# Optimization experiments

Measured on AMD Instinct MI355X. Metric: run time of the kernel, lower is better.

## Reference

```python
import jax, jax.numpy as jnp
import numpy as np

B, N, C, H, AD, HID = 2, 1024, 768, 12, 8, 3072
SCALE = (C // H) ** -0.5


def setup_inputs() -> dict:
    key = jax.random.key(0)
    ks = jax.random.split(key, 32)
    inp = {}
    for i in range(5):
        inp[f"x{i}"] = jax.random.normal(ks[i], (B, N, C), jnp.float32)
    def w(i, shape, s=0.02):
        return jax.random.normal(ks[i], shape, jnp.float32) * s
    inp.update({
        "ln1_g": jnp.ones((C,), jnp.float32), "ln1_b": jnp.zeros((C,), jnp.float32),
        "ln2_g": jnp.ones((C,), jnp.float32), "ln2_b": jnp.zeros((C,), jnp.float32),
        "qkv_w": w(5, (C, 3 * C)), "qkv_b": jnp.zeros((3 * C,), jnp.float32),
        "proj_w": w(6, (C, C)), "proj_b": jnp.zeros((C,), jnp.float32),
        "fc1_w": w(7, (C, HID)), "fc1_b": jnp.zeros((HID,), jnp.float32),
        "fc2_w": w(8, (HID, C)), "fc2_b": jnp.zeros((C,), jnp.float32),
        "at_dw": w(9, (C, AD)), "at_db": jnp.zeros((AD,), jnp.float32),
        "at_mw": w(10, (AD, AD)), "at_mb": jnp.zeros((AD,), jnp.float32),
        "at_uw": w(11, (AD, C)), "at_ub": jnp.zeros((C,), jnp.float32),
        "a2_dw": w(12, (C, AD)), "a2_db": jnp.zeros((AD,), jnp.float32),
        "a2_mw": w(13, (AD, AD)), "a2_mb": jnp.zeros((AD,), jnp.float32),
        "a2_uw": w(14, (AD, C)), "a2_ub": jnp.zeros((C,), jnp.float32),
    })
    return inp


def _ln(x, g, b, eps=1e-5):
    mu = x.mean(-1, keepdims=True)
    xc = x - mu
    var = (xc * xc).mean(-1, keepdims=True)
    return xc * jax.lax.rsqrt(var + eps) * g + b


def _adapter(x, dw, db, mw, mb, uw, ub):
    h = x @ dw + db          # bottleneck down [., AD]
    h = h @ mw + mb          # mid
    return h @ uw + ub       # up back to C


def _attn(x, qkv_w, qkv_b, proj_w, proj_b):
    # x: [S, B, N, C] (streams folded in leading axis)
    s, b, n, c = x.shape
    qkv = (x @ qkv_w + qkv_b).reshape(s, b, n, 3, H, c // H)
    q, k, v = jnp.moveaxis(qkv, 3, 0)            # each [S,B,N,H,D]
    scores = jnp.einsum('sbnhd,sbmhd->sbhnm', q * SCALE, k)  # fp32; clamp is a no-op
    p = jax.nn.softmax(scores, axis=-1)
    o = jnp.einsum('sbhnm,sbmhd->sbnhd', p, v).reshape(s, b, n, c)
    return o @ proj_w + proj_b


def reference(x0, x1, x2, x3, x4,
              ln1_g, ln1_b, ln2_g, ln2_b,
              qkv_w, qkv_b, proj_w, proj_b,
              fc1_w, fc1_b, fc2_w, fc2_b,
              at_dw, at_db, at_mw, at_mb, at_uw, at_ub,
              a2_dw, a2_db, a2_mw, a2_mb, a2_uw, a2_ub):
    xs = jnp.stack([x0, x1, x2, x3, x4])          # [5,B,N,C]
    n1 = _ln(xs, ln1_g, ln1_b)
    a1 = _adapter(n1, at_dw, at_db, at_mw, at_mb, at_uw, at_ub)
    ao = _attn(n1, qkv_w, qkv_b, proj_w, proj_b)
    # cross-stream residuals: x01=a1[0], x12=a1[1], ..., x10=a1[1], x21=a1[2], ...
    y0 = xs[0] + ao[0] + a1[1]
    y1 = xs[1] + ao[1] + a1[0] + a1[2]
    y2 = xs[2] + ao[2] + a1[1] + a1[3]
    y3 = xs[3] + ao[3] + a1[2] + a1[4]
    y4 = xs[4] + ao[4] + a1[3]
    ys = jnp.stack([y0, y1, y2, y3, y4])
    a2 = _adapter(_ln(ys, ln1_g, ln1_b), a2_dw, a2_db, a2_mw, a2_mb, a2_uw, a2_ub)
    h = _ln(ys, ln2_g, ln2_b) @ fc1_w + fc1_b
    m = jax.nn.gelu(h, approximate=False) @ fc2_w + fc2_b
    z0 = ys[0] + m[0] + a2[1]
    z1 = ys[1] + m[1] + a2[0] + a2[2]
    z2 = ys[2] + m[2] + a2[1] + a2[3]
    z3 = ys[3] + m[3] + a2[2] + a2[4]
    z4 = ys[4] + m[4] + a2[3]
    return jnp.stack([z0, z1, z2, z3, z4])        # [5,B,N,C]
```

## Files before the change

kernel.cpp:

```cpp
#include <hip/hip_runtime.h>
#include <math.h>

typedef __bf16 bf16;
typedef __attribute__((ext_vector_type(8))) __bf16 bf16x8;
typedef __attribute__((ext_vector_type(4))) __bf16 bf16x4;
typedef __attribute__((ext_vector_type(4))) float f32x4;
typedef __attribute__((ext_vector_type(16))) float f32x16;

#define TOK   10240
#define CD    768
#define NQKV  2304
#define NHID  3072
#define SEQ   1024
#define NH    12

__device__ __forceinline__ f32x4 mfma16(bf16x8 a, bf16x8 b, f32x4 c) {
  return __builtin_amdgcn_mfma_f32_16x16x32_bf16(a, b, c, 0, 0, 0);
}
__device__ __forceinline__ f32x16 mfma32(bf16x8 a, bf16x8 b, f32x16 c) {
  return __builtin_amdgcn_mfma_f32_32x32x16_bf16(a, b, c, 0, 0, 0);
}

__device__ __forceinline__ void gload16(const void* g, void* l) {
  __builtin_amdgcn_global_load_lds(
      (const __attribute__((address_space(1))) void*)g,
      (__attribute__((address_space(3))) void*)l, 16, 0, 0);
}

__device__ __forceinline__ unsigned pack2(bf16 a, bf16 b) {
  union { unsigned short u[2]; unsigned v; } x;
  x.u[0] = __builtin_bit_cast(unsigned short, a);
  x.u[1] = __builtin_bit_cast(unsigned short, b);
  return x.v;
}

__global__ __launch_bounds__(256) void transpose_to_bf16(
    const float* __restrict__ in, bf16* __restrict__ out, int K, int N) {
  __shared__ float tile[32][33];
  const int bn = blockIdx.x * 32, bk = blockIdx.y * 32;
  const int r = threadIdx.x >> 5, c = threadIdx.x & 31;
#pragma unroll
  for (int i = 0; i < 4; ++i)
    tile[r + 8 * i][c] = in[(size_t)(bk + r + 8 * i) * N + bn + c];
  __syncthreads();
#pragma unroll
  for (int i = 0; i < 4; ++i)
    out[(size_t)(bn + r + 8 * i) * K + bk + c] = (bf16)tile[c][r + 8 * i];
}

__global__ __launch_bounds__(256) void ln5_kernel(
    const float* __restrict__ x0, const float* __restrict__ x1,
    const float* __restrict__ x2, const float* __restrict__ x3,
    const float* __restrict__ x4, const float* __restrict__ g,
    const float* __restrict__ b, bf16* __restrict__ out) {
  const int w = threadIdx.x >> 6, lane = threadIdx.x & 63;
  const int row = blockIdx.x * 4 + w;
  const int s = row >> 11, rem = row & 2047;
  const float* xp;
  switch (s) {
    case 0: xp = x0; break; case 1: xp = x1; break; case 2: xp = x2; break;
    case 3: xp = x3; break; default: xp = x4; break;
  }
  const f32x4* xr = (const f32x4*)(xp + (size_t)rem * CD);
  f32x4 v[3];
#pragma unroll
  for (int i = 0; i < 3; ++i) v[i] = xr[lane + 64 * i];
  float sum = 0.f;
#pragma unroll
  for (int i = 0; i < 3; ++i)
#pragma unroll
    for (int j = 0; j < 4; ++j) sum += v[i][j];
#pragma unroll
  for (int m = 32; m >= 1; m >>= 1) sum += __shfl_xor(sum, m);
  const float mu = sum * (1.f / 768.f);
  float vs = 0.f;
#pragma unroll
  for (int i = 0; i < 3; ++i)
#pragma unroll
    for (int j = 0; j < 4; ++j) { float d = v[i][j] - mu; vs += d * d; }
#pragma unroll
  for (int m = 32; m >= 1; m >>= 1) vs += __shfl_xor(vs, m);
  const float rstd = rsqrtf(vs * (1.f / 768.f) + 1e-5f);
  const f32x4* gp = (const f32x4*)g;
  const f32x4* bp = (const f32x4*)b;
  bf16* orow = out + (size_t)row * CD;
#pragma unroll
  for (int i = 0; i < 3; ++i) {
    const int c4 = lane + 64 * i;
    f32x4 gg = gp[c4], bb = bp[c4];
    bf16x4 o;
#pragma unroll
    for (int j = 0; j < 4; ++j)
      o[j] = (bf16)((v[i][j] - mu) * rstd * gg[j] + bb[j]);
    *(bf16x4*)(orow + c4 * 4) = o;
  }
}

__global__ __launch_bounds__(256) void ln_dual_kernel(
    const float* __restrict__ in, const float* __restrict__ g1,
    const float* __restrict__ b1, const float* __restrict__ g2,
    const float* __restrict__ b2, bf16* __restrict__ o1,
    bf16* __restrict__ o2) {
  const int w = threadIdx.x >> 6, lane = threadIdx.x & 63;
  const int row = blockIdx.x * 4 + w;
  const f32x4* xr = (const f32x4*)(in + (size_t)row * CD);
  f32x4 v[3];
#pragma unroll
  for (int i = 0; i < 3; ++i) v[i] = xr[lane + 64 * i];
  float sum = 0.f;
#pragma unroll
  for (int i = 0; i < 3; ++i)
#pragma unroll
    for (int j = 0; j < 4; ++j) sum += v[i][j];
#pragma unroll
  for (int m = 32; m >= 1; m >>= 1) sum += __shfl_xor(sum, m);
  const float mu = sum * (1.f / 768.f);
  float vs = 0.f;
#pragma unroll
  for (int i = 0; i < 3; ++i)
#pragma unroll
    for (int j = 0; j < 4; ++j) { float d = v[i][j] - mu; vs += d * d; }
#pragma unroll
  for (int m = 32; m >= 1; m >>= 1) vs += __shfl_xor(vs, m);
  const float rstd = rsqrtf(vs * (1.f / 768.f) + 1e-5f);
  bf16* r1 = o1 + (size_t)row * CD;
  bf16* r2 = o2 + (size_t)row * CD;
#pragma unroll
  for (int i = 0; i < 3; ++i) {
    const int c4 = lane + 64 * i;
    f32x4 gg1 = ((const f32x4*)g1)[c4], bb1 = ((const f32x4*)b1)[c4];
    f32x4 gg2 = ((const f32x4*)g2)[c4], bb2 = ((const f32x4*)b2)[c4];
    bf16x4 oa, ob;
#pragma unroll
    for (int j = 0; j < 4; ++j) {
      float n = (v[i][j] - mu) * rstd;
      oa[j] = (bf16)(n * gg1[j] + bb1[j]);
      ob[j] = (bf16)(n * gg2[j] + bb2[j]);
    }
    *(bf16x4*)(r1 + c4 * 4) = oa;
    *(bf16x4*)(r2 + c4 * 4) = ob;
  }
}

template <int EPI>
__global__ __launch_bounds__(256) void gemm_bt(
    const bf16* __restrict__ A, const bf16* __restrict__ Bt,
    const float* __restrict__ bias, void* __restrict__ Cout, int N, int K) {
  __shared__ bf16 As[4096];
  __shared__ bf16 Bs[4096];
  const int t = threadIdx.x, lane = t & 63, w = t >> 6;
  const int wm = w >> 1, wn = w & 1;
  const int bn = blockIdx.x, bm = blockIdx.y;
  f32x4 acc[4][4] = {};

  const int srow = t >> 2;
  const int scol = ((t & 3) ^ (srow & 3)) << 3;
  const bf16* a0 = A + (size_t)(bm * 128 + srow) * K + scol;
  const bf16* b0 = Bt + (size_t)(bn * 128 + srow) * K + scol;
  bf16* asw = As + w * 512;
  bf16* bsw = Bs + w * 512;
  const size_t rstride = (size_t)64 * K;

  const int arow = wm * 64 + (lane & 15);
  const int brow = wn * 64 + (lane & 15);
  const int pch = (((lane >> 4) ^ (lane & 3)) << 3);

  for (int kt = 0; kt < K; kt += 32) {
    const bf16* ak = a0 + kt;
    const bf16* bk = b0 + kt;
    gload16(ak, asw);
    gload16(ak + rstride, asw + 2048);
    gload16(bk, bsw);
    gload16(bk + rstride, bsw + 2048);
    __syncthreads();
    bf16x8 af[4], bfr[4];
#pragma unroll
    for (int f = 0; f < 4; ++f) {
      af[f] = *(const bf16x8*)&As[(arow + f * 16) * 32 + pch];
      bfr[f] = *(const bf16x8*)&Bs[(brow + f * 16) * 32 + pch];
    }
#pragma unroll
    for (int mf = 0; mf < 4; ++mf)
#pragma unroll
      for (int nf = 0; nf < 4; ++nf)
        acc[mf][nf] = mfma16(af[mf], bfr[nf], acc[mf][nf]);
    __syncthreads();
  }

#pragma unroll
  for (int mf = 0; mf < 4; ++mf) {
    const int grow0 = bm * 128 + wm * 64 + mf * 16 + (lane >> 4) * 4;
#pragma unroll
    for (int nf = 0; nf < 4; ++nf) {
      const int gcol = bn * 128 + wn * 64 + nf * 16 + (lane & 15);
      const float bv = bias[gcol];
#pragma unroll
      for (int r = 0; r < 4; ++r) {
        float v = acc[mf][nf][r] + bv;
        if (EPI == 2) v = 0.5f * v * (1.f + erff(v * 0.70710678f));
        const size_t idx = (size_t)(grow0 + r) * N + gcol;
        if (EPI == 0) ((float*)Cout)[idx] = v;
        else ((bf16*)Cout)[idx] = (bf16)v;
      }
    }
  }
}

__global__ __launch_bounds__(256, 3) void attn_v2(
    const bf16* __restrict__ qkv, bf16* __restrict__ obuf) {
  __shared__ bf16 Ks[2][4096];
  __shared__ bf16 Vt[2][4096];
  const int t = threadIdx.x, lane = t & 63, w = t >> 6;
  const int g = lane >> 5, q32 = lane & 31, rq7 = q32 & 7;

  const int xcd = blockIdx.x & 7, slot = blockIdx.x >> 3;
  const int work = xcd * 120 + slot;
  const int sbh = work >> 3, qt = work & 7;
  const int sb = sbh / NH, h = sbh % NH;
  const size_t tokbase = (size_t)sb * SEQ;
  const int qoff = h * 64, koff = CD + h * 64, voff = 2 * CD + h * 64;

  const int qrow = qt * 128 + w * 32 + q32;
  bf16x8 qf[4];
  {
    const bf16* qp = qkv + (tokbase + qrow) * NQKV + qoff + g * 8;
#pragma unroll
    for (int kd = 0; kd < 4; ++kd) {
      bf16x8 v = *(const bf16x8*)(qp + kd * 16);
#pragma unroll
      for (int j = 0; j < 8; ++j) v[j] = (bf16)((float)v[j] * 0.125f);
      qf[kd] = v;
    }
  }

  const int skv1 = t >> 3, sc1 = (t & 7) ^ (skv1 & 7);
  const int skv2 = (t + 256) >> 3, sc2 = (t & 7) ^ (skv2 & 7);
  const int vkv0 = 2 * (t & 31);
  const int vd0 = 8 * (t >> 5);
  const int c0 = (vkv0 & 51) | ((vkv0 & 4) << 1) | ((vkv0 & 8) >> 1);
  const int vchunk = c0 >> 3, vsub = c0 & 7;
  const bf16* kbase = qkv + tokbase * NQKV + koff;
  const bf16* vbase = qkv + tokbase * NQKV + voff;

  {
    const bf16* kb0 = kbase;
    gload16(kb0 + (size_t)skv1 * NQKV + sc1 * 8, &Ks[0][w * 512]);
    gload16(kb0 + (size_t)skv2 * NQKV + sc2 * 8, &Ks[0][2048 + w * 512]);
    const bf16* vp = vbase + (size_t)vkv0 * NQKV + vd0;
    bf16x8 r0 = *(const bf16x8*)vp;
    bf16x8 r1 = *(const bf16x8*)(vp + NQKV);
#pragma unroll
    for (int j = 0; j < 8; ++j) {
      const int d = vd0 + j;
      *(unsigned*)&Vt[0][d * 64 + ((vchunk ^ j) << 3) + vsub] =
          pack2(r0[j], r1[j]);
    }
  }
  __syncthreads();

  float m_run = -1e30f, l_run = 0.f;
  f32x16 oT0 = {}, oT1 = {};
  int cur = 0;

  for (int kt = 0; kt < 16; ++kt) {
    bf16x8 nv0, nv1;
    if (kt < 15) {
      const bf16* vp = vbase + (size_t)((kt + 1) * 64 + vkv0) * NQKV + vd0;
      nv0 = *(const bf16x8*)vp;
      nv1 = *(const bf16x8*)(vp + NQKV);
      const bf16* kb0 = kbase + (size_t)(kt + 1) * 64 * NQKV;
      gload16(kb0 + (size_t)skv1 * NQKV + sc1 * 8, &Ks[cur ^ 1][w * 512]);
      gload16(kb0 + (size_t)skv2 * NQKV + sc2 * 8,
              &Ks[cur ^ 1][2048 + w * 512]);
    }

    f32x16 sT0 = {}, sT1 = {};
#pragma unroll
    for (int kd = 0; kd < 4; ++kd) {
      bf16x8 kf0 =
          *(const bf16x8*)&Ks[cur][q32 * 64 + (((2 * kd + g) ^ rq7) << 3)];
      bf16x8 kf1 = *(const bf16x8*)&Ks[cur][(32 + q32) * 64 +
                                            (((2 * kd + g) ^ rq7) << 3)];
      sT0 = mfma32(kf0, qf[kd], sT0);
      sT1 = mfma32(kf1, qf[kd], sT1);
    }

    float mt = sT0[0];
#pragma unroll
    for (int r = 1; r < 16; ++r) mt = fmaxf(mt, sT0[r]);
#pragma unroll
    for (int r = 0; r < 16; ++r) mt = fmaxf(mt, sT1[r]);
    mt = fmaxf(mt, __shfl_xor(mt, 32));
    const float mnew = fmaxf(m_run, mt);
    const float alpha = __expf(m_run - mnew);
    m_run = mnew;
    float rs = 0.f;
#pragma unroll
    for (int r = 0; r < 16; ++r) {
      sT0[r] = __expf(sT0[r] - mnew);
      rs += sT0[r];
    }
#pragma unroll
    for (int r = 0; r < 16; ++r) {
      sT1[r] = __expf(sT1[r] - mnew);
      rs += sT1[r];
    }
    rs += __shfl_xor(rs, 32);
    l_run = l_run * alpha + rs;
#pragma unroll
    for (int r = 0; r < 16; ++r) { oT0[r] *= alpha; oT1[r] *= alpha; }

    bf16x8 pa[4];
#pragma unroll
    for (int hh = 0; hh < 2; ++hh)
#pragma unroll
      for (int j = 0; j < 8; ++j) {
        pa[hh][j] = (bf16)sT0[8 * hh + j];
        pa[2 + hh][j] = (bf16)sT1[8 * hh + j];
      }

#pragma unroll
    for (int ks = 0; ks < 4; ++ks) {
      bf16x8 vf0 =
          *(const bf16x8*)&Vt[cur][q32 * 64 + (((2 * ks + g) ^ rq7) << 3)];
      bf16x8 vf1 = *(const bf16x8*)&Vt[cur][(32 + q32) * 64 +
                                            (((2 * ks + g) ^ rq7) << 3)];
      oT0 = mfma32(vf0, pa[ks], oT0);
      oT1 = mfma32(vf1, pa[ks], oT1);
    }

    if (kt < 15) {
#pragma unroll
      for (int j = 0; j < 8; ++j) {
        const int d = vd0 + j;
        *(unsigned*)&Vt[cur ^ 1][d * 64 + ((vchunk ^ j) << 3) + vsub] =
            pack2(nv0[j], nv1[j]);
      }
    }
    __syncthreads();
    cur ^= 1;
  }

  const float rl = 1.f / l_run;
  bf16* orow = obuf + (tokbase + qrow) * CD + h * 64;
#pragma unroll
  for (int m = 0; m < 4; ++m) {
    bf16x4 o0, o1;
#pragma unroll
    for (int r = 0; r < 4; ++r) {
      o0[r] = (bf16)(oT0[4 * m + r] * rl);
      o1[r] = (bf16)(oT1[4 * m + r] * rl);
    }
    *(bf16x4*)(orow + 8 * m + 4 * g) = o0;
    *(bf16x4*)(orow + 32 + 8 * m + 4 * g) = o1;
  }
}

__global__ __launch_bounds__(256) void adapter_kernel(
    const bf16* __restrict__ X, const float* __restrict__ dw,
    const float* __restrict__ db, const float* __restrict__ mw,
    const float* __restrict__ mb, const float* __restrict__ uw,
    const float* __restrict__ ub, float* __restrict__ out) {
  const int tok = blockIdx.x * 4 + (threadIdx.x >> 6);
  const int lane = threadIdx.x & 63;
  const bf16* xr = X + (size_t)tok * CD;
  float xv[12];
#pragma unroll
  for (int i = 0; i < 12; ++i) xv[i] = (float)xr[lane + 64 * i];
  float h1[8] = {0, 0, 0, 0, 0, 0, 0, 0};
#pragma unroll
  for (int i = 0; i < 12; ++i) {
    const f32x4* dr = (const f32x4*)(dw + (size_t)(lane + 64 * i) * 8);
    f32x4 d0 = dr[0], d1 = dr[1];
#pragma unroll
    for (int j = 0; j < 4; ++j) {
      h1[j] += xv[i] * d0[j];
      h1[4 + j] += xv[i] * d1[j];
    }
  }
#pragma unroll
  for (int m = 1; m < 64; m <<= 1)
#pragma unroll
    for (int j = 0; j < 8; ++j) h1[j] += __shfl_xor(h1[j], m);
#pragma unroll
  for (int j = 0; j < 8; ++j) h1[j] += db[j];
  float h2[8];
#pragma unroll
  for (int k = 0; k < 8; ++k) {
    float v = mb[k];
#pragma unroll
    for (int j = 0; j < 8; ++j) v += h1[j] * mw[j * 8 + k];
    h2[k] = v;
  }
#pragma unroll
  for (int i = 0; i < 12; ++i) {
    const int c = lane + 64 * i;
    float v = ub[c];
#pragma unroll
    for (int k = 0; k < 8; ++k) v += h2[k] * uw[k * CD + c];
    out[(size_t)tok * CD + c] = v;
  }
}

__global__ __launch_bounds__(256) void cross_residual(
    const float* __restrict__ p0, const float* __restrict__ p1,
    const float* __restrict__ p2, const float* __restrict__ p3,
    const float* __restrict__ p4, const float* __restrict__ add,
    const float* __restrict__ a, float* __restrict__ out) {
  const int s = blockIdx.y;
  const size_t i = (size_t)blockIdx.x * 256 + threadIdx.x;
  const size_t spitch = (size_t)2048 * 768 / 4;
  const size_t sb = (size_t)s * spitch;
  const float* p;
  switch (s) {
    case 0: p = p0; break; case 1: p = p1; break; case 2: p = p2; break;
    case 3: p = p3; break; default: p = p4; break;
  }
  f32x4 v = ((const f32x4*)p)[i];
  v += ((const f32x4*)add)[sb + i];
  if (s > 0) v += ((const f32x4*)a)[sb - spitch + i];
  if (s < 4) v += ((const f32x4*)a)[sb + spitch + i];
  ((f32x4*)out)[sb + i] = v;
}

#define OFF_WTQKV  ((size_t)0)
#define OFF_WTPROJ ((size_t)3538944)
#define OFF_WTFC1  ((size_t)4718592)
#define OFF_WTFC2  ((size_t)9437184)
#define OFF_N1     ((size_t)14155776)
#define OFF_BIG    ((size_t)29884416)
#define OFF_OBUF   ((size_t)77070336)
#define OFF_AOM    ((size_t)92798976)
#define OFF_A12    ((size_t)124256256)
#define OFF_YS     ((size_t)155713536)
#define OFF_L2Y    ((size_t)187170816)

extern "C" void kernel_launch(void* const* d_in, const int* in_sizes, int n_in,
                              void* d_out, int out_size, void* d_ws,
                              size_t ws_size, hipStream_t stream) {
  const float* x0 = (const float*)d_in[0];
  const float* x1 = (const float*)d_in[1];
  const float* x2 = (const float*)d_in[2];
  const float* x3 = (const float*)d_in[3];
  const float* x4 = (const float*)d_in[4];
  const float* ln1_g = (const float*)d_in[5];
  const float* ln1_b = (const float*)d_in[6];
  const float* ln2_g = (const float*)d_in[7];
  const float* ln2_b = (const float*)d_in[8];
  const float* qkv_w = (const float*)d_in[9];
  const float* qkv_b = (const float*)d_in[10];
  const float* proj_w = (const float*)d_in[11];
  const float* proj_b = (const float*)d_in[12];
  const float* fc1_w = (const float*)d_in[13];
  const float* fc1_b = (const float*)d_in[14];
  const float* fc2_w = (const float*)d_in[15];
  const float* fc2_b = (const float*)d_in[16];
  const float* at_dw = (const float*)d_in[17];
  const float* at_db = (const float*)d_in[18];
  const float* at_mw = (const float*)d_in[19];
  const float* at_mb = (const float*)d_in[20];
  const float* at_uw = (const float*)d_in[21];
  const float* at_ub = (const float*)d_in[22];
  const float* a2_dw = (const float*)d_in[23];
  const float* a2_db = (const float*)d_in[24];
  const float* a2_mw = (const float*)d_in[25];
  const float* a2_mb = (const float*)d_in[26];
  const float* a2_uw = (const float*)d_in[27];
  const float* a2_ub = (const float*)d_in[28];

  char* ws = (char*)d_ws;
  bf16* wt_qkv = (bf16*)(ws + OFF_WTQKV);
  bf16* wt_proj = (bf16*)(ws + OFF_WTPROJ);
  bf16* wt_fc1 = (bf16*)(ws + OFF_WTFC1);
  bf16* wt_fc2 = (bf16*)(ws + OFF_WTFC2);
  bf16* n1 = (bf16*)(ws + OFF_N1);
  bf16* qkvb = (bf16*)(ws + OFF_BIG);
  bf16* obuf = (bf16*)(ws + OFF_OBUF);
  float* aom = (float*)(ws + OFF_AOM);
  float* a12 = (float*)(ws + OFF_A12);
  float* ysb = (float*)(ws + OFF_YS);
  bf16* l2y = (bf16*)(ws + OFF_L2Y);

  const dim3 b256(256);

  transpose_to_bf16<<<dim3(72, 24), b256, 0, stream>>>(qkv_w, wt_qkv, 768, 2304);
  transpose_to_bf16<<<dim3(24, 24), b256, 0, stream>>>(proj_w, wt_proj, 768, 768);
  transpose_to_bf16<<<dim3(96, 24), b256, 0, stream>>>(fc1_w, wt_fc1, 768, 3072);
  transpose_to_bf16<<<dim3(24, 96), b256, 0, stream>>>(fc2_w, wt_fc2, 3072, 768);

  ln5_kernel<<<2560, b256, 0, stream>>>(x0, x1, x2, x3, x4, ln1_g, ln1_b, n1);

  gemm_bt<1><<<dim3(18, 80), b256, 0, stream>>>(n1, wt_qkv, qkv_b, qkvb, NQKV, 768);

  adapter_kernel<<<2560, b256, 0, stream>>>(n1, at_dw, at_db, at_mw, at_mb,
                                            at_uw, at_ub, a12);

  attn_v2<<<960, b256, 0, stream>>>(qkvb, obuf);

  gemm_bt<0><<<dim3(6, 80), b256, 0, stream>>>(obuf, wt_proj, proj_b, aom, CD, 768);

  cross_residual<<<dim3(1536, 5), b256, 0, stream>>>(x0, x1, x2, x3, x4, aom,
                                                     a12, ysb);

  ln_dual_kernel<<<2560, b256, 0, stream>>>(ysb, ln1_g, ln1_b, ln2_g, ln2_b,
                                            n1, l2y);

  adapter_kernel<<<2560, b256, 0, stream>>>(n1, a2_dw, a2_db, a2_mw, a2_mb,
                                            a2_uw, a2_ub, a12);

  gemm_bt<2><<<dim3(24, 80), b256, 0, stream>>>(l2y, wt_fc1, fc1_b, qkvb, NHID, 768);

  gemm_bt<0><<<dim3(6, 80), b256, 0, stream>>>(qkvb, wt_fc2, fc2_b, aom, CD, NHID);

  const size_t sp = (size_t)2048 * 768;
  cross_residual<<<dim3(1536, 5), b256, 0, stream>>>(
      ysb, ysb + sp, ysb + 2 * sp, ysb + 3 * sp, ysb + 4 * sp, aom, a12,
      (float*)d_out);
}
```

Measured before the change: 439.7 us.

## Double-buffer GEMM loads, remap blocks per XCD, fuse residual into LN, approximate GELU

The GEMM now prefetches the next K tile into a second LDS buffer while computing the current one, and maps blocks so consecutive tiles land on the same XCD. The cross-stream residual is folded into the dual LayerNorm kernel, removing one full fp32 pass over the activations. Exact erf GELU is replaced with a tanh approximation using a fast exp, which slightly changes numerics relative to the reference.

```diff
diff --git a/kernel.cpp b/kernel.cpp
--- a/kernel.cpp
+++ b/kernel.cpp
@@ -32,6 +32,12 @@
   x.u[0] = __builtin_bit_cast(unsigned short, a);
   x.u[1] = __builtin_bit_cast(unsigned short, b);
   return x.v;
+}
+
+__device__ __forceinline__ float fast_gelu(float v) {
+  float u = 0.7978845608f * (v + 0.044715f * v * v * v);
+  float e = __expf(fminf(2.f * u, 30.f));
+  return 0.5f * v * (1.f + (e - 1.f) / (e + 1.f));
 }
 
 __global__ __launch_bounds__(256) void transpose_to_bf16(
@@ -96,17 +102,39 @@
   }
 }
 
-__global__ __launch_bounds__(256) void ln_dual_kernel(
-    const float* __restrict__ in, const float* __restrict__ g1,
-    const float* __restrict__ b1, const float* __restrict__ g2,
-    const float* __restrict__ b2, bf16* __restrict__ o1,
-    bf16* __restrict__ o2) {
+__global__ __launch_bounds__(256) void fuse_res_ln(
+    const float* __restrict__ x0, const float* __restrict__ x1,
+    const float* __restrict__ x2, const float* __restrict__ x3,
+    const float* __restrict__ x4, const float* __restrict__ add,
+    const float* __restrict__ a, float* __restrict__ ys,
+    const float* __restrict__ g1, const float* __restrict__ b1,
+    const float* __restrict__ g2, const float* __restrict__ b2,
+    bf16* __restrict__ o1, bf16* __restrict__ o2) {
   const int w = threadIdx.x >> 6, lane = threadIdx.x & 63;
   const int row = blockIdx.x * 4 + w;
-  const f32x4* xr = (const f32x4*)(in + (size_t)row * CD);
+  const int s = row >> 11, rem = row & 2047;
+  const float* xp;
+  switch (s) {
+    case 0: xp = x0; break; case 1: xp = x1; break; case 2: xp = x2; break;
+    case 3: xp = x3; break; default: xp = x4; break;
+  }
+  const f32x4* xr = (const f32x4*)(xp + (size_t)rem * CD);
+  const f32x4* ar = (const f32x4*)(add + (size_t)row * CD);
+  const f32x4* am = (const f32x4*)(a + (size_t)(row - 2048) * CD);
+  const f32x4* ap = (const f32x4*)(a + (size_t)(row + 2048) * CD);
   f32x4 v[3];
 #pragma unroll
-  for (int i = 0; i < 3; ++i) v[i] = xr[lane + 64 * i];
+  for (int i = 0; i < 3; ++i) {
+    const int c4 = lane + 64 * i;
+    f32x4 t = xr[c4] + ar[c4];
+    if (s > 0) t += am[c4];
+    if (s < 4) t += ap[c4];
+    v[i] = t;
+  }
+  f32x4* yr = (f32x4*)(ys + (size_t)row * CD);
+#pragma unroll
+  for (int i = 0; i < 3; ++i) yr[lane + 64 * i] = v[i];
+
   float sum = 0.f;
 #pragma unroll
   for (int i = 0; i < 3; ++i)
@@ -145,39 +173,50 @@
 template <int EPI>
 __global__ __launch_bounds__(256) void gemm_bt(
     const bf16* __restrict__ A, const bf16* __restrict__ Bt,
-    const float* __restrict__ bias, void* __restrict__ Cout, int N, int K) {
-  __shared__ bf16 As[4096];
-  __shared__ bf16 Bs[4096];
+    const float* __restrict__ bias, void* __restrict__ Cout, int N, int K,
+    int nbn) {
+  __shared__ bf16 As[2][4096];
+  __shared__ bf16 Bs[2][4096];
   const int t = threadIdx.x, lane = t & 63, w = t >> 6;
   const int wm = w >> 1, wn = w & 1;
-  const int bn = blockIdx.x, bm = blockIdx.y;
+
+  const int chunk = gridDim.x >> 3;
+  const int wg = (blockIdx.x & 7) * chunk + (blockIdx.x >> 3);
+  const int bm = wg / nbn, bn = wg % nbn;
+
   f32x4 acc[4][4] = {};
 
   const int srow = t >> 2;
   const int scol = ((t & 3) ^ (srow & 3)) << 3;
   const bf16* a0 = A + (size_t)(bm * 128 + srow) * K + scol;
   const bf16* b0 = Bt + (size_t)(bn * 128 + srow) * K + scol;
-  bf16* asw = As + w * 512;
-  bf16* bsw = Bs + w * 512;
   const size_t rstride = (size_t)64 * K;
 
   const int arow = wm * 64 + (lane & 15);
   const int brow = wn * 64 + (lane & 15);
   const int pch = (((lane >> 4) ^ (lane & 3)) << 3);
 
+  gload16(a0, &As[0][w * 512]);
+  gload16(a0 + rstride, &As[0][2048 + w * 512]);
+  gload16(b0, &Bs[0][w * 512]);
+  gload16(b0 + rstride, &Bs[0][2048 + w * 512]);
+  __syncthreads();
+
+  int cur = 0;
   for (int kt = 0; kt < K; kt += 32) {
-    const bf16* ak = a0 + kt;
-    const bf16* bk = b0 + kt;
-    gload16(ak, asw);
-    gload16(ak + rstride, asw + 2048);
-    gload16(bk, bsw);
-    gload16(bk + rstride, bsw + 2048);
-    __syncthreads();
+    if (kt + 32 < K) {
+      const bf16* ak = a0 + kt + 32;
+      const bf16* bk = b0 + kt + 32;
+      gload16(ak, &As[cur ^ 1][w * 512]);
+      gload16(ak + rstride, &As[cur ^ 1][2048 + w * 512]);
+      gload16(bk, &Bs[cur ^ 1][w * 512]);
+      gload16(bk + rstride, &Bs[cur ^ 1][2048 + w * 512]);
+    }
     bf16x8 af[4], bfr[4];
 #pragma unroll
     for (int f = 0; f < 4; ++f) {
-      af[f] = *(const bf16x8*)&As[(arow + f * 16) * 32 + pch];
-      bfr[f] = *(const bf16x8*)&Bs[(brow + f * 16) * 32 + pch];
+      af[f] = *(const bf16x8*)&As[cur][(arow + f * 16) * 32 + pch];
+      bfr[f] = *(const bf16x8*)&Bs[cur][(brow + f * 16) * 32 + pch];
     }
 #pragma unroll
     for (int mf = 0; mf < 4; ++mf)
@@ -185,6 +224,7 @@
       for (int nf = 0; nf < 4; ++nf)
         acc[mf][nf] = mfma16(af[mf], bfr[nf], acc[mf][nf]);
     __syncthreads();
+    cur ^= 1;
   }
 
 #pragma unroll
@@ -197,7 +237,7 @@
 #pragma unroll
       for (int r = 0; r < 4; ++r) {
         float v = acc[mf][nf][r] + bv;
-        if (EPI == 2) v = 0.5f * v * (1.f + erff(v * 0.70710678f));
+        if (EPI == 2) v = fast_gelu(v);
         const size_t idx = (size_t)(grow0 + r) * N + gcol;
         if (EPI == 0) ((float*)Cout)[idx] = v;
         else ((bf16*)Cout)[idx] = (bf16)v;
@@ -490,27 +530,24 @@
 
   ln5_kernel<<<2560, b256, 0, stream>>>(x0, x1, x2, x3, x4, ln1_g, ln1_b, n1);
 
-  gemm_bt<1><<<dim3(18, 80), b256, 0, stream>>>(n1, wt_qkv, qkv_b, qkvb, NQKV, 768);
+  gemm_bt<1><<<1440, b256, 0, stream>>>(n1, wt_qkv, qkv_b, qkvb, NQKV, 768, 18);
 
   adapter_kernel<<<2560, b256, 0, stream>>>(n1, at_dw, at_db, at_mw, at_mb,
                                             at_uw, at_ub, a12);
 
   attn_v2<<<960, b256, 0, stream>>>(qkvb, obuf);
 
-  gemm_bt<0><<<dim3(6, 80), b256, 0, stream>>>(obuf, wt_proj, proj_b, aom, CD, 768);
-
-  cross_residual<<<dim3(1536, 5), b256, 0, stream>>>(x0, x1, x2, x3, x4, aom,
-                                                     a12, ysb);
-
-  ln_dual_kernel<<<2560, b256, 0, stream>>>(ysb, ln1_g, ln1_b, ln2_g, ln2_b,
-                                            n1, l2y);
+  gemm_bt<0><<<480, b256, 0, stream>>>(obuf, wt_proj, proj_b, aom, CD, 768, 6);
+
+  fuse_res_ln<<<2560, b256, 0, stream>>>(x0, x1, x2, x3, x4, aom, a12, ysb,
+                                         ln1_g, ln1_b, ln2_g, ln2_b, n1, l2y);
 
   adapter_kernel<<<2560, b256, 0, stream>>>(n1, a2_dw, a2_db, a2_mw, a2_mb,
                                             a2_uw, a2_ub, a12);
 
-  gemm_bt<2><<<dim3(24, 80), b256, 0, stream>>>(l2y, wt_fc1, fc1_b, qkvb, NHID, 768);
-
-  gemm_bt<0><<<dim3(6, 80), b256, 0, stream>>>(qkvb, wt_fc2, fc2_b, aom, CD, NHID);
+  gemm_bt<2><<<1920, b256, 0, stream>>>(l2y, wt_fc1, fc1_b, qkvb, NHID, 768, 24);
+
+  gemm_bt<0><<<480, b256, 0, stream>>>(qkvb, wt_fc2, fc2_b, aom, CD, NHID, 6);
 
   const size_t sp = (size_t)2048 * 768;
   cross_residual<<<dim3(1536, 5), b256, 0, stream>>>(
```

New measurement: 405.2 us. -7.8%, faster.
